# Optimization experiments

Hardware: AMD Instinct MI355X
Metric: run time of the kernel (lower is better)

Reference implementation:

```python
import jax, jax.numpy as jnp
import numpy as np

B, C, S, D = 4, 16, 512, 512
H = 8
HD = D // H
FFN = 2048
MAX_WL = 10000.0
ROPE_PCT = 0.5
EPS = 1e-5


def setup_inputs() -> dict:
    key = jax.random.key(0)
    ks = jax.random.split(key, 8)
    w = lambda k, shape: jax.random.normal(k, shape, jnp.float32) * 0.02
    return {
        "x": jax.random.normal(ks[0], (B, C, S, D), jnp.float32),
        "Wq": w(ks[1], (D, D)), "bq": jnp.zeros((D,), jnp.float32),
        "Wk": w(ks[2], (D, D)), "bk": jnp.zeros((D,), jnp.float32),
        "Wv": w(ks[3], (D, D)), "bv": jnp.zeros((D,), jnp.float32),
        "Wo": w(ks[4], (D, D)), "bo": jnp.zeros((D,), jnp.float32),
        "ln1_g": jnp.ones((D,), jnp.float32), "ln1_b": jnp.zeros((D,), jnp.float32),
        "ln3_g": jnp.ones((D,), jnp.float32), "ln3_b": jnp.zeros((D,), jnp.float32),
        "W1": w(ks[5], (D, FFN)), "b1": jnp.zeros((FFN,), jnp.float32),
        "W2": w(ks[6], (FFN, D)), "b2": jnp.zeros((D,), jnp.float32),
    }


def _layernorm(x, g, b):
    mu = jnp.mean(x, axis=-1, keepdims=True)
    var = jnp.mean((x - mu) ** 2, axis=-1, keepdims=True)
    return (x - mu) * jax.lax.rsqrt(var + EPS) * g + b


def _p_rope(x, pos):
    # partial rotary: rotate first ROPE_PCT fraction of rotation angles, pass rest through
    half = HD // 2
    rope_angles = int(ROPE_PCT * HD) // 2  # 16 for HD=64, pct=0.5
    exps = (2.0 / HD) * jnp.arange(rope_angles, dtype=jnp.float32)
    timescale = MAX_WL ** exps
    timescale = jnp.concatenate([timescale, jnp.full((half - rope_angles,), jnp.inf, jnp.float32)])
    ang = pos[:, None] / timescale[None, :]  # (S, half); inf timescale -> angle 0 -> identity
    sin, cos = jnp.sin(ang), jnp.cos(ang)
    x1, x2 = x[..., :half], x[..., half:]
    return jnp.concatenate([x1 * cos - x2 * sin, x2 * cos + x1 * sin], axis=-1)


def _forward(x, Wq, bq, Wk, bk, Wv, bv, Wo, bo, ln1_g, ln1_b, ln3_g, ln3_b, W1, b1, W2, b2):
    h = x.reshape(B * C, S, D)
    # --- temporal self-attention (pre-norm) ---
    hn = _layernorm(h, ln1_g, ln1_b)
    scaling = HD ** -0.5
    q = (hn @ Wq + bq) * scaling
    k = hn @ Wk + bk
    v = hn @ Wv + bv
    split = lambda t: t.reshape(B * C, S, H, HD).transpose(0, 2, 1, 3)  # (BC,H,S,HD)
    q, k, v = split(q), split(k), split(v)
    pos = jnp.arange(S, dtype=jnp.float32)
    q = _p_rope(q, pos)
    k = _p_rope(k, pos)
    attn = jax.nn.softmax(jnp.einsum('bhqd,bhkd->bhqk', q, k), axis=-1)
    o = jnp.einsum('bhqk,bhkd->bhqd', attn, v)
    o = o.transpose(0, 2, 1, 3).reshape(B * C, S, D) @ Wo + bo
    h = h + o
    # --- feed-forward (pre-norm) ---
    hn = _layernorm(h, ln3_g, ln3_b)
    ff = jax.nn.gelu(hn @ W1 + b1, approximate=False) @ W2 + b2
    h = h + ff
    return h.reshape(B, C, S, D)


def reference(x, Wq, bq, Wk, bk, Wv, bv, Wo, bo, ln1_g, ln1_b, ln3_g, ln3_b, W1, b1, W2, b2):
    return _forward(x, Wq, bq, Wk, bk, Wv, bv, Wo, bo, ln1_g, ln1_b, ln3_g, ln3_b, W1, b1, W2, b2)
```

## Files before the change

kernel.cpp:

```cpp
#include <hip/hip_runtime.h>
#include <math.h>

typedef unsigned short u16;
typedef __attribute__((ext_vector_type(8))) short bf16x8;
typedef __attribute__((ext_vector_type(4))) float f32x4;

#define MFMA16(a, b, c) __builtin_amdgcn_mfma_f32_16x16x32_bf16((a), (b), (c), 0, 0, 0)

__device__ __forceinline__ u16 f2bf(float f) {
    union { float f; unsigned u; } v; v.f = f;
    unsigned u = v.u;
    unsigned r = (u + 0x7FFFu + ((u >> 16) & 1u)) >> 16;
    return (u16)r;
}

__device__ __forceinline__ unsigned pack_bf16(float lo, float hi) {
    union { float f; unsigned u; } a, b; a.f = lo; b.f = hi;
    return __builtin_amdgcn_perm(b.u + 0x8000u, a.u + 0x8000u, 0x07060302u);
}

__device__ __forceinline__ float fexp2(float x) {
#if __has_builtin(__builtin_amdgcn_exp2f)
    return __builtin_amdgcn_exp2f(x);
#else
    return __expf(x * 0.6931471805599453f);
#endif
}

__device__ __forceinline__ void gl_lds16(const u16* g, u16* l) {
    __builtin_amdgcn_global_load_lds(
        (const __attribute__((address_space(1))) unsigned*)g,
        (__attribute__((address_space(3))) unsigned*)l, 16, 0, 0);
}

__global__ __launch_bounds__(256) void transpose_cvt_all(
    const float* __restrict__ Wq, const float* __restrict__ Wk,
    const float* __restrict__ Wv, const float* __restrict__ Wo,
    const float* __restrict__ W1, const float* __restrict__ W2,
    u16* __restrict__ wqt, u16* __restrict__ wkt, u16* __restrict__ wvt,
    u16* __restrict__ wot, u16* __restrict__ w1t, u16* __restrict__ w2t)
{
    __shared__ float tile[64][65];
    int fb = blockIdx.x;
    const float* src; u16* dst; int K, N, bx, by;
    if (fb < 256) {
        int w = fb >> 6, b = fb & 63;
        src = (w == 0) ? Wq : (w == 1) ? Wk : (w == 2) ? Wv : Wo;
        dst = (w == 0) ? wqt : (w == 1) ? wkt : (w == 2) ? wvt : wot;
        K = 512; N = 512; bx = b & 7; by = b >> 3;
    } else if (fb < 512) {
        int b = fb - 256; src = W1; dst = w1t; K = 512; N = 2048; bx = b & 31; by = b >> 5;
    } else {
        int b = fb - 512; src = W2; dst = w2t; K = 2048; N = 512; bx = b & 7; by = b >> 3;
    }
    int n0 = bx * 64, k0 = by * 64;
    int tx = threadIdx.x & 63, ty = threadIdx.x >> 6;
    #pragma unroll
    for (int i = ty; i < 64; i += 4)
        tile[i][tx] = src[(size_t)(k0 + i) * N + n0 + tx];
    __syncthreads();
    #pragma unroll
    for (int i = ty; i < 64; i += 4)
        dst[(size_t)(n0 + i) * K + k0 + tx] = f2bf(tile[tx][i]);
}

__global__ __launch_bounds__(256) void ln_kernel(const float* __restrict__ in,
                                                 u16* __restrict__ out,
                                                 const float* __restrict__ g,
                                                 const float* __restrict__ b) {
    int row = blockIdx.x;
    const float* rp = in + (size_t)row * 512;
    int t = threadIdx.x;
    float2 v = *(const float2*)(rp + t * 2);
    float s = v.x + v.y;
    float sq = v.x * v.x + v.y * v.y;
    #pragma unroll
    for (int off = 32; off > 0; off >>= 1) {
        s  += __shfl_down(s, off, 64);
        sq += __shfl_down(sq, off, 64);
    }
    __shared__ float red[8];
    __shared__ float stat[2];
    int wid = t >> 6;
    if ((t & 63) == 0) { red[wid] = s; red[wid + 4] = sq; }
    __syncthreads();
    if (t == 0) {
        float S = red[0] + red[1] + red[2] + red[3];
        float Q = red[4] + red[5] + red[6] + red[7];
        float mu = S * (1.0f / 512.0f);
        float var = Q * (1.0f / 512.0f) - mu * mu;
        stat[0] = mu;
        stat[1] = rsqrtf(var + 1e-5f);
    }
    __syncthreads();
    float mu = stat[0], inv = stat[1];
    int c = t * 2;
    float2 gv = *(const float2*)(g + c);
    float2 bv = *(const float2*)(b + c);
    ushort2 ov;
    ov.x = f2bf((v.x - mu) * inv * gv.x + bv.x);
    ov.y = f2bf((v.y - mu) * inv * gv.y + bv.y);
    *(ushort2*)(out + (size_t)row * 512 + c) = ov;
}


#define BAR()   __builtin_amdgcn_s_barrier()
#define LGKM0() asm volatile("s_waitcnt lgkmcnt(0)" ::: "memory")
#define VM6()   asm volatile("s_waitcnt vmcnt(6)" ::: "memory")
#define PRIO1() __builtin_amdgcn_s_setprio(1)
#define PRIO0() __builtin_amdgcn_s_setprio(0)

__device__ __forceinline__ bf16x8 ldfrag(const u16* __restrict__ base, int R, int ko, int lq) {
    int o = (ko + lq * 8) ^ ((R & 7) * 8);
    return *(const bf16x8*)(base + R * 64 + o);
}

__device__ __forceinline__ void stage_half(const u16* __restrict__ g, int ldk,
                                           u16* __restrict__ dst, int t) {
    #pragma unroll
    for (int p = 0; p < 2; ++p) {
        int idx = p * 512 + t;
        int row = idx >> 3;
        int col = ((idx & 7) * 8) ^ ((row & 7) * 8);
        gl_lds16(g + (size_t)row * ldk + col, dst + idx * 8);
    }
}

__device__ __forceinline__ void gemm256_core(
    const u16* __restrict__ A, const u16* __restrict__ Bt, int K,
    int m0, int n0, int t, u16* __restrict__ smem, f32x4 (&acc)[8][4])
{
    const int NS = K >> 6;
    const int wid = t >> 6, lane = t & 63;
    const int lm = lane & 15, lq = lane >> 4;
    const int wm_ = wid >> 2;
    const int wn_ = wid & 3;
    const int wbh = wn_ >> 1;
    const int wbr = (wn_ & 1) * 64;

    auto reg = [&](int buf, int ab, int half) -> u16* {
        return smem + (((buf << 1) | ab) * 2 + half) * 8192;
    };
    auto stage = [&](int h) {
        int u = h >> 2;
        if (u >= NS) return;
        int w = h & 3;
        int k0 = u << 6, buf = u & 1;
        if (w < 2)
            stage_half(Bt + (size_t)(n0 + w * 128) * K + k0, K, reg(buf, 1, w), t);
        else
            stage_half(A + (size_t)(m0 + (w - 2) * 128) * K + k0, K, reg(buf, 0, w - 2), t);
    };

    #pragma unroll
    for (int i = 0; i < 8; ++i)
        #pragma unroll
        for (int j = 0; j < 4; ++j) acc[i][j] = (f32x4){0.f, 0.f, 0.f, 0.f};

    #pragma unroll
    for (int h = 0; h < 7; ++h) stage(h);
    VM6();
    BAR();

    for (int s = 0; s < NS; ++s) {
        const u16* As = reg(s & 1, 0, wm_);
        const u16* Bs = reg(s & 1, 1, wbh);
        bf16x8 aF[4][2], bF[4][2];
        #pragma unroll
        for (int i = 0; i < 4; ++i) {
            aF[i][0] = ldfrag(As, i * 16 + lm, 0, lq);
            aF[i][1] = ldfrag(As, i * 16 + lm, 32, lq);
        }
        #pragma unroll
        for (int j = 0; j < 4; ++j) {
            bF[j][0] = ldfrag(Bs, wbr + j * 16 + lm, 0, lq);
            bF[j][1] = ldfrag(Bs, wbr + j * 16 + lm, 32, lq);
        }
        stage(4 * (s + 1) + 3);
        BAR(); LGKM0(); PRIO1();
        #pragma unroll
        for (int i = 0; i < 4; ++i)
            #pragma unroll
            for (int j = 0; j < 2; ++j) {
                acc[i][j] = MFMA16(aF[i][0], bF[j][0], acc[i][j]);
                acc[i][j] = MFMA16(aF[i][1], bF[j][1], acc[i][j]);
            }
        PRIO0(); BAR();
        stage(4 * (s + 2) + 0);
        BAR(); LGKM0(); PRIO1();
        #pragma unroll
        for (int i = 0; i < 4; ++i)
            #pragma unroll
            for (int j = 0; j < 2; ++j) {
                acc[i][2 + j] = MFMA16(aF[i][0], bF[2 + j][0], acc[i][2 + j]);
                acc[i][2 + j] = MFMA16(aF[i][1], bF[2 + j][1], acc[i][2 + j]);
            }
        PRIO0(); BAR();
        #pragma unroll
        for (int i = 0; i < 4; ++i) {
            aF[i][0] = ldfrag(As, 64 + i * 16 + lm, 0, lq);
            aF[i][1] = ldfrag(As, 64 + i * 16 + lm, 32, lq);
        }
        stage(4 * (s + 2) + 1);
        BAR(); LGKM0(); PRIO1();
        #pragma unroll
        for (int i = 0; i < 4; ++i)
            #pragma unroll
            for (int j = 0; j < 2; ++j) {
                acc[4 + i][j] = MFMA16(aF[i][0], bF[j][0], acc[4 + i][j]);
                acc[4 + i][j] = MFMA16(aF[i][1], bF[j][1], acc[4 + i][j]);
            }
        PRIO0(); BAR();
        stage(4 * (s + 2) + 2);
        BAR(); LGKM0(); PRIO1();
        #pragma unroll
        for (int i = 0; i < 4; ++i)
            #pragma unroll
            for (int j = 0; j < 2; ++j) {
                acc[4 + i][2 + j] = MFMA16(aF[i][0], bF[2 + j][0], acc[4 + i][2 + j]);
                acc[4 + i][2 + j] = MFMA16(aF[i][1], bF[2 + j][1], acc[4 + i][2 + j]);
            }
        PRIO0();
        VM6();
        BAR();
    }
}

__global__ __launch_bounds__(512) void qkv256_kernel(
    const u16* __restrict__ A,
    const u16* __restrict__ wqt, const u16* __restrict__ wkt, const u16* __restrict__ wvt,
    const float* __restrict__ bqp, const float* __restrict__ bkp, const float* __restrict__ bvp,
    u16* __restrict__ qb, u16* __restrict__ kb, u16* __restrict__ vb, float sclq)
{
    __shared__ u16 smem[65536];
    int flat = blockIdx.x;
    int xcd = flat & 7, slot = flat >> 3;
    int g = xcd * 96 + slot;
    int mt = g / 6, nt = g % 6;
    int mode = nt >> 1;
    int m0 = mt * 256, nb0 = (nt & 1) * 256;
    const u16* Bt = (mode == 0) ? wqt : (mode == 1) ? wkt : wvt;
    const float* bias = (mode == 0) ? bqp : (mode == 1) ? bkp : bvp;
    u16* outp = (mode == 0) ? qb : (mode == 1) ? kb : vb;

    int t = threadIdx.x;
    f32x4 acc[8][4];
    gemm256_core(A, Bt, 512, m0, nb0, t, smem, acc);

    int wid = t >> 6, lane = t & 63, lm = lane & 15, lq = lane >> 4;
    int rowb = m0 + (wid >> 2) * 128;
    int colb = nb0 + (wid & 3) * 64;

    if (mode < 2) {
        float bv0 = bias[colb + 0 * 16 + lm];
        float bv1 = bias[colb + 1 * 16 + lm];
        float bv2 = bias[colb + 2 * 16 + lm];
        float bv3 = bias[colb + 3 * 16 + lm];
        float its = __expf((float)lm * -0.28782313662425572f);
        float scl = (mode == 0) ? sclq : 1.f;
        #pragma unroll
        for (int i = 0; i < 8; ++i) {
            #pragma unroll
            for (int r = 0; r < 4; ++r) {
                int gm = rowb + i * 16 + lq * 4 + r;
                int s = gm & 511;
                float ang = (float)s * its;
                float sn = __sinf(ang), cs = __cosf(ang);
                float x1 = acc[i][0][r] + bv0;
                float x2 = acc[i][2][r] + bv2;
                float y0 = (x1 * cs - x2 * sn) * scl;
                float y2 = (x2 * cs + x1 * sn) * scl;
                float y1 = (acc[i][1][r] + bv1) * scl;
                float y3 = (acc[i][3][r] + bv3) * scl;
                size_t base = ((size_t)(gm >> 9)) * 262144 + (size_t)(colb >> 6) * 32768
                            + (size_t)s * 64 + lm;
                outp[base +  0] = f2bf(y0);
                outp[base + 16] = f2bf(y1);
                outp[base + 32] = f2bf(y2);
                outp[base + 48] = f2bf(y3);
            }
        }
    } else {
        #pragma unroll
        for (int i = 0; i < 8; ++i)
            #pragma unroll
            for (int j = 0; j < 4; ++j) {
                int gn = colb + j * 16 + lm;
                float bvv = bias[gn];
                #pragma unroll
                for (int r = 0; r < 4; ++r) {
                    int gm = rowb + i * 16 + lq * 4 + r;
                    float v = acc[i][j][r] + bvv;
                    size_t idx = ((size_t)(gm >> 9)) * 262144 + (size_t)(gn >> 6) * 32768
                               + (size_t)(gn & 63) * 512 + (gm & 511);
                    outp[idx] = f2bf(v);
                }
            }
    }
}

template<int MODE>
__global__ __launch_bounds__(512) void gemm256_kernel(
    const u16* __restrict__ A, const u16* __restrict__ Bt,
    const float* __restrict__ bias, const float* __restrict__ res,
    void* __restrict__ outp, int M, int N, int K)
{
    __shared__ u16 smem[65536];
    int flat = blockIdx.x;
    int nbt = N >> 8;
    int nwg = (M >> 8) * nbt;
    int xcd = flat & 7, slot = flat >> 3;
    int g = xcd * (nwg >> 3) + slot;
    int mt = g / nbt, nt = g % nbt;
    int m0 = mt * 256, n0 = nt * 256;

    int t = threadIdx.x;
    f32x4 acc[8][4];
    gemm256_core(A, Bt, K, m0, n0, t, smem, acc);

    int wid = t >> 6, lane = t & 63, lm = lane & 15, lq = lane >> 4;
    int rowb = m0 + (wid >> 2) * 128, colb = n0 + (wid & 3) * 64;
    #pragma unroll
    for (int i = 0; i < 8; ++i)
        #pragma unroll
        for (int j = 0; j < 4; ++j) {
            int gn = colb + j * 16 + lm;
            float bv = bias[gn];
            #pragma unroll
            for (int r = 0; r < 4; ++r) {
                int gm = rowb + i * 16 + lq * 4 + r;
                float v = acc[i][j][r] + bv;
                if (MODE == 3) {
                    size_t idx = (size_t)gm * N + gn;
                    ((float*)outp)[idx] = v + res[idx];
                } else {
                    float gl = 0.5f * v * (1.f + erff(v * 0.70710678118654752f));
                    ((u16*)outp)[(size_t)gm * N + gn] = f2bf(gl);
                }
            }
        }
}

__global__ __launch_bounds__(256) void attn_kernel(
    const u16* __restrict__ q, const u16* __restrict__ k,
    const u16* __restrict__ vt, u16* __restrict__ o)
{
    int flat = blockIdx.y * gridDim.x + blockIdx.x;
    int xcd = flat & 7, slot = flat >> 3;
    int nh = xcd * 64 + (slot >> 1);
    int qt = slot & 1;
    const u16* Qb = q + (size_t)nh * 32768 + (size_t)qt * 16384;
    const u16* Kb = k + (size_t)nh * 32768;
    const u16* Vb = vt + (size_t)nh * 32768;
    __shared__ u16 lK[64][72], lV[64][72];
    __shared__ u16 lP[4][16][72];
    int t = threadIdx.x, wid = t >> 6, lane = t & 63, lm = lane & 15, lq = lane >> 4;

    bf16x8 bq[4][2];
    #pragma unroll
    for (int sub = 0; sub < 4; ++sub) {
        const u16* qr = Qb + (size_t)(sub * 64 + wid * 16 + lm) * 64;
        bq[sub][0] = *(const bf16x8*)(qr + lq * 8);
        bq[sub][1] = *(const bf16x8*)(qr + 32 + lq * 8);
    }

    const f32x4 zero = {0.f, 0.f, 0.f, 0.f};
    f32x4 Oacc[4][4];
    float mo[4], l[4];
    #pragma unroll
    for (int s = 0; s < 4; ++s) {
        mo[s] = -INFINITY; l[s] = 0.f;
        #pragma unroll
        for (int d = 0; d < 4; ++d) Oacc[s][d] = zero;
    }

    for (int kt = 0; kt < 8; ++kt) {
        #pragma unroll
        for (int p = 0; p < 2; ++p) {
            int idx = p * 256 + t, row = idx >> 3, ch = (idx & 7) * 8;
            *(uint4*)&lK[row][ch] = *(const uint4*)(Kb + (size_t)(kt * 64 + row) * 64 + ch);
            *(uint4*)&lV[row][ch] = *(const uint4*)(Vb + (size_t)row * 512 + kt * 64 + ch);
        }
        __syncthreads();
        bf16x8 aK[4][2], aV[4][2];
        #pragma unroll
        for (int i = 0; i < 4; ++i) {
            aK[i][0] = *(const bf16x8*)&lK[i * 16 + lm][lq * 8];
            aK[i][1] = *(const bf16x8*)&lK[i * 16 + lm][32 + lq * 8];
            aV[i][0] = *(const bf16x8*)&lV[i * 16 + lm][lq * 8];
            aV[i][1] = *(const bf16x8*)&lV[i * 16 + lm][32 + lq * 8];
        }
        #pragma unroll
        for (int sub = 0; sub < 4; ++sub) {
            f32x4 sc[4];
            #pragma unroll
            for (int i = 0; i < 4; ++i) {
                f32x4 z = MFMA16(aK[i][0], bq[sub][0], zero);
                sc[i] = MFMA16(aK[i][1], bq[sub][1], z);
            }
            float mx = sc[0][0];
            #pragma unroll
            for (int i = 0; i < 4; ++i)
                #pragma unroll
                for (int r = 0; r < 4; ++r) mx = fmaxf(mx, sc[i][r]);
            mx = fmaxf(mx, __shfl_xor(mx, 16, 64));
            mx = fmaxf(mx, __shfl_xor(mx, 32, 64));
            float mn = fmaxf(mo[sub], mx);
            float al = fexp2(mo[sub] - mn);
            float pv[4][4], sum = 0.f;
            #pragma unroll
            for (int i = 0; i < 4; ++i)
                #pragma unroll
                for (int r = 0; r < 4; ++r) { pv[i][r] = fexp2(sc[i][r] - mn); sum += pv[i][r]; }
            sum += __shfl_xor(sum, 16, 64);
            sum += __shfl_xor(sum, 32, 64);
            l[sub] = l[sub] * al + sum;
            mo[sub] = mn;
            #pragma unroll
            for (int dn = 0; dn < 4; ++dn) Oacc[sub][dn] *= al;
            #pragma unroll
            for (int i = 0; i < 4; ++i) {
                uint2 w2;
                w2.x = pack_bf16(pv[i][0], pv[i][1]);
                w2.y = pack_bf16(pv[i][2], pv[i][3]);
                *(uint2*)&lP[wid][lm][i * 16 + lq * 4] = w2;
            }
            bf16x8 bp0 = *(const bf16x8*)&lP[wid][lm][lq * 8];
            bf16x8 bp1 = *(const bf16x8*)&lP[wid][lm][32 + lq * 8];
            #pragma unroll
            for (int dn = 0; dn < 4; ++dn) {
                Oacc[sub][dn] = MFMA16(aV[dn][0], bp0, Oacc[sub][dn]);
                Oacc[sub][dn] = MFMA16(aV[dn][1], bp1, Oacc[sub][dn]);
            }
        }
        __syncthreads();
    }
    int bc = nh >> 3, h = nh & 7;
    #pragma unroll
    for (int sub = 0; sub < 4; ++sub) {
        float inv = 1.f / l[sub];
        size_t orow = ((size_t)(bc * 512 + qt * 256 + sub * 64 + wid * 16 + lm)) * 512 + h * 64;
        #pragma unroll
        for (int dn = 0; dn < 4; ++dn) {
            uint2 w2;
            w2.x = pack_bf16(Oacc[sub][dn][0] * inv, Oacc[sub][dn][1] * inv);
            w2.y = pack_bf16(Oacc[sub][dn][2] * inv, Oacc[sub][dn][3] * inv);
            *(uint2*)(o + orow + dn * 16 + lq * 4) = w2;
        }
    }
}

extern "C" void kernel_launch(void* const* d_in, const int* in_sizes, int n_in,
                              void* d_out, int out_size, void* d_ws, size_t ws_size,
                              hipStream_t stream) {
    const float* x    = (const float*)d_in[0];
    const float* Wq   = (const float*)d_in[1];
    const float* bq   = (const float*)d_in[2];
    const float* Wk   = (const float*)d_in[3];
    const float* bk   = (const float*)d_in[4];
    const float* Wv   = (const float*)d_in[5];
    const float* bv   = (const float*)d_in[6];
    const float* Wo   = (const float*)d_in[7];
    const float* bo   = (const float*)d_in[8];
    const float* ln1g = (const float*)d_in[9];
    const float* ln1b = (const float*)d_in[10];
    const float* ln3g = (const float*)d_in[11];
    const float* ln3b = (const float*)d_in[12];
    const float* W1   = (const float*)d_in[13];
    const float* b1   = (const float*)d_in[14];
    const float* W2   = (const float*)d_in[15];
    const float* b2   = (const float*)d_in[16];

    char* ws = (char*)d_ws;
    u16*  hn  = (u16*)(ws + 0ull);
    u16*  qb  = (u16*)(ws + 33554432ull);
    u16*  kb  = (u16*)(ws + 67108864ull);
    u16*  vb  = (u16*)(ws + 100663296ull);
    u16*  ob  = (u16*)(ws + 134217728ull);
    u16*  ffa = (u16*)(ws + 33554432ull);
    float* h1 = (float*)(ws + 167772160ull);
    u16*  wqt = (u16*)(ws + 234881024ull);
    u16*  wkt = (u16*)(ws + 235405312ull);
    u16*  wvt = (u16*)(ws + 235929600ull);
    u16*  wot = (u16*)(ws + 236453888ull);
    u16*  w1t = (u16*)(ws + 236978176ull);
    u16*  w2t = (u16*)(ws + 239075328ull);

    dim3 blk(256);
    transpose_cvt_all<<<768, blk, 0, stream>>>(Wq, Wk, Wv, Wo, W1, W2,
                                               wqt, wkt, wvt, wot, w1t, w2t);

    ln_kernel<<<32768, blk, 0, stream>>>(x, hn, ln1g, ln1b);

    qkv256_kernel<<<768, dim3(512), 0, stream>>>(hn, wqt, wkt, wvt, bq, bk, bv,
                                                 qb, kb, vb,
                                                 0.125f * 1.4426950408889634f);

    attn_kernel<<<dim3(2, 512), blk, 0, stream>>>(qb, kb, vb, ob);

    gemm256_kernel<3><<<256, dim3(512), 0, stream>>>(ob, wot, bo, x, h1,
                                                     32768, 512, 512);

    ln_kernel<<<32768, blk, 0, stream>>>(h1, hn, ln3g, ln3b);

    gemm256_kernel<4><<<1024, dim3(512), 0, stream>>>(hn, w1t, b1, nullptr, ffa,
                                                      32768, 2048, 512);
    gemm256_kernel<3><<<256, dim3(512), 0, stream>>>(ffa, w2t, b2, h1,
                                                     (float*)d_out, 32768, 512, 2048);
}
```

Before: 600.2 us.

## Restructure GEMM K-loop into k-half phases with precomputed staging addresses

Reorganizes the 256x256 GEMM main loop so each phase loads only one 32-wide k-slice of A and B fragments and runs 16 MFMAs across all four B column tiles. The old four-way column/row split held both k-halves live. The prefetch schedule changes: A for the next stage and B two stages ahead are issued in halves, with vmcnt(4), falling back to vmcnt(0) in the tail. Global staging addresses are now precomputed once per thread instead of being recomputed per call. The aim is lower register pressure and address arithmetic, plus better copy/compute overlap, at the cost of a riskier, more fragile synchronization schedule.

```diff
diff --git a/kernel.cpp b/kernel.cpp
--- a/kernel.cpp
+++ b/kernel.cpp
@@ -104,26 +104,17 @@
 }
 
 
-#define BAR()   __builtin_amdgcn_s_barrier()
+#define FENCE() asm volatile("" ::: "memory")
+#define BARF()  do { FENCE(); __builtin_amdgcn_s_barrier(); FENCE(); } while (0)
 #define LGKM0() asm volatile("s_waitcnt lgkmcnt(0)" ::: "memory")
-#define VM6()   asm volatile("s_waitcnt vmcnt(6)" ::: "memory")
+#define VM4()   asm volatile("s_waitcnt vmcnt(4)" ::: "memory")
+#define VM0()   asm volatile("s_waitcnt vmcnt(0)" ::: "memory")
 #define PRIO1() __builtin_amdgcn_s_setprio(1)
 #define PRIO0() __builtin_amdgcn_s_setprio(0)
 
 __device__ __forceinline__ bf16x8 ldfrag(const u16* __restrict__ base, int R, int ko, int lq) {
     int o = (ko + lq * 8) ^ ((R & 7) * 8);
     return *(const bf16x8*)(base + R * 64 + o);
-}
-
-__device__ __forceinline__ void stage_half(const u16* __restrict__ g, int ldk,
-                                           u16* __restrict__ dst, int t) {
-    #pragma unroll
-    for (int p = 0; p < 2; ++p) {
-        int idx = p * 512 + t;
-        int row = idx >> 3;
-        int col = ((idx & 7) * 8) ^ ((row & 7) * 8);
-        gl_lds16(g + (size_t)row * ldk + col, dst + idx * 8);
-    }
 }
 
 __device__ __forceinline__ void gemm256_core(
@@ -141,88 +132,89 @@
     auto reg = [&](int buf, int ab, int half) -> u16* {
         return smem + (((buf << 1) | ab) * 2 + half) * 8192;
     };
-    auto stage = [&](int h) {
-        int u = h >> 2;
+
+    const int r0 = t >> 3;
+    const int csw = ((t & 7) * 8) ^ ((r0 & 7) * 8);
+    const u16* gA = A + (size_t)(m0 + r0) * K + csw;
+    const u16* gB = Bt + (size_t)(n0 + r0) * K + csw;
+    const size_t pK64 = (size_t)64 * K;
+    const size_t hK128 = (size_t)128 * K;
+
+    auto stA = [&](int u, int hf) {
         if (u >= NS) return;
-        int w = h & 3;
-        int k0 = u << 6, buf = u & 1;
-        if (w < 2)
-            stage_half(Bt + (size_t)(n0 + w * 128) * K + k0, K, reg(buf, 1, w), t);
-        else
-            stage_half(A + (size_t)(m0 + (w - 2) * 128) * K + k0, K, reg(buf, 0, w - 2), t);
+        u16* d = reg(u & 1, 0, hf) + t * 8;
+        const u16* s = gA + (size_t)(u * 64) + (hf ? hK128 : (size_t)0);
+        gl_lds16(s, d);
+        gl_lds16(s + pK64, d + 4096);
     };
+    auto stB = [&](int u, int hf) {
+        if (u >= NS) return;
+        u16* d = reg(u & 1, 1, hf) + t * 8;
+        const u16* s = gB + (size_t)(u * 64) + (hf ? hK128 : (size_t)0);
+        gl_lds16(s, d);
+        gl_lds16(s + pK64, d + 4096);
+    };
 
     #pragma unroll
     for (int i = 0; i < 8; ++i)
         #pragma unroll
         for (int j = 0; j < 4; ++j) acc[i][j] = (f32x4){0.f, 0.f, 0.f, 0.f};
 
-    #pragma unroll
-    for (int h = 0; h < 7; ++h) stage(h);
-    VM6();
-    BAR();
+    stB(0, 0); stB(0, 1); stA(0, 0); stA(0, 1);
+    stB(1, 0); stB(1, 1);
+    VM4();
+    BARF();
 
     for (int s = 0; s < NS; ++s) {
         const u16* As = reg(s & 1, 0, wm_);
         const u16* Bs = reg(s & 1, 1, wbh);
-        bf16x8 aF[4][2], bF[4][2];
-        #pragma unroll
-        for (int i = 0; i < 4; ++i) {
-            aF[i][0] = ldfrag(As, i * 16 + lm, 0, lq);
-            aF[i][1] = ldfrag(As, i * 16 + lm, 32, lq);
-        }
-        #pragma unroll
-        for (int j = 0; j < 4; ++j) {
-            bF[j][0] = ldfrag(Bs, wbr + j * 16 + lm, 0, lq);
-            bF[j][1] = ldfrag(Bs, wbr + j * 16 + lm, 32, lq);
-        }
-        stage(4 * (s + 1) + 3);
-        BAR(); LGKM0(); PRIO1();
+        bf16x8 aF[4], bF[4][2];
+        #pragma unroll
+        for (int i = 0; i < 4; ++i) aF[i] = ldfrag(As, i * 16 + lm, 0, lq);
+        #pragma unroll
+        for (int j = 0; j < 4; ++j) bF[j][0] = ldfrag(Bs, wbr + j * 16 + lm, 0, lq);
+        stA(s + 1, 0);
+        BARF(); PRIO1();
         #pragma unroll
         for (int i = 0; i < 4; ++i)
             #pragma unroll
-            for (int j = 0; j < 2; ++j) {
-                acc[i][j] = MFMA16(aF[i][0], bF[j][0], acc[i][j]);
-                acc[i][j] = MFMA16(aF[i][1], bF[j][1], acc[i][j]);
-            }
-        PRIO0(); BAR();
-        stage(4 * (s + 2) + 0);
-        BAR(); LGKM0(); PRIO1();
+            for (int j = 0; j < 4; ++j)
+                acc[i][j] = MFMA16(aF[i], bF[j][0], acc[i][j]);
+        PRIO0(); LGKM0(); BARF();
+        #pragma unroll
+        for (int i = 0; i < 4; ++i) aF[i] = ldfrag(As, i * 16 + lm, 32, lq);
+        #pragma unroll
+        for (int j = 0; j < 4; ++j) bF[j][1] = ldfrag(Bs, wbr + j * 16 + lm, 32, lq);
+        stA(s + 1, 1);
+        BARF(); PRIO1();
         #pragma unroll
         for (int i = 0; i < 4; ++i)
             #pragma unroll
-            for (int j = 0; j < 2; ++j) {
-                acc[i][2 + j] = MFMA16(aF[i][0], bF[2 + j][0], acc[i][2 + j]);
-                acc[i][2 + j] = MFMA16(aF[i][1], bF[2 + j][1], acc[i][2 + j]);
-            }
-        PRIO0(); BAR();
-        #pragma unroll
-        for (int i = 0; i < 4; ++i) {
-            aF[i][0] = ldfrag(As, 64 + i * 16 + lm, 0, lq);
-            aF[i][1] = ldfrag(As, 64 + i * 16 + lm, 32, lq);
-        }
-        stage(4 * (s + 2) + 1);
-        BAR(); LGKM0(); PRIO1();
+            for (int j = 0; j < 4; ++j)
+                acc[i][j] = MFMA16(aF[i], bF[j][1], acc[i][j]);
+        PRIO0(); LGKM0(); BARF();
+        #pragma unroll
+        for (int i = 0; i < 4; ++i) aF[i] = ldfrag(As, 64 + i * 16 + lm, 0, lq);
+        stB(s + 2, 0);
+        BARF(); PRIO1();
         #pragma unroll
         for (int i = 0; i < 4; ++i)
             #pragma unroll
-            for (int j = 0; j < 2; ++j) {
-                acc[4 + i][j] = MFMA16(aF[i][0], bF[j][0], acc[4 + i][j]);
-                acc[4 + i][j] = MFMA16(aF[i][1], bF[j][1], acc[4 + i][j]);
-            }
-        PRIO0(); BAR();
-        stage(4 * (s + 2) + 2);
-        BAR(); LGKM0(); PRIO1();
+            for (int j = 0; j < 4; ++j)
+                acc[4 + i][j] = MFMA16(aF[i], bF[j][0], acc[4 + i][j]);
+        PRIO0(); LGKM0(); BARF();
+        #pragma unroll
+        for (int i = 0; i < 4; ++i) aF[i] = ldfrag(As, 64 + i * 16 + lm, 32, lq);
+        stB(s + 2, 1);
+        BARF(); PRIO1();
         #pragma unroll
         for (int i = 0; i < 4; ++i)
             #pragma unroll
-            for (int j = 0; j < 2; ++j) {
-                acc[4 + i][2 + j] = MFMA16(aF[i][0], bF[2 + j][0], acc[4 + i][2 + j]);
-                acc[4 + i][2 + j] = MFMA16(aF[i][1], bF[2 + j][1], acc[4 + i][2 + j]);
-            }
-        PRIO0();
-        VM6();
-        BAR();
+            for (int j = 0; j < 4; ++j)
+                acc[4 + i][j] = MFMA16(aF[i], bF[j][1], acc[4 + i][j]);
+        PRIO0(); LGKM0();
+        if (s >= NS - 2) { VM0(); } else { VM4(); }
+        BARF();
     }
 }
 
```

Result: no change. 602.2 us (+0.3%).
